# Performance work log

Hardware: AMD Instinct MI355X
Metric: run time of the kernel (lower is better)

Reference implementation:

```python
import jax, jax.numpy as jnp
import numpy as np

IDIM = 1024
HIDDEN = 4096
N_EXPERT = 8
T = 2048


def setup_inputs() -> dict:
    key = jax.random.key(0)
    ks = jax.random.split(key, 6)
    s_in = 1.0 / np.sqrt(IDIM)
    s_h = 1.0 / np.sqrt(HIDDEN)
    return {
        "xs": jax.random.normal(ks[0], (T, IDIM), dtype=jnp.float32),
        "top_k": 2,
        # gate: Linear(idim -> n_expert, bias=False); torch weight (E, D)
        "Wg": jax.random.uniform(ks[1], (N_EXPERT, IDIM), jnp.float32, -s_in, s_in),
        # experts stacked: w_1 Linear(idim->hidden), w_2 Linear(hidden->idim)
        "W1": jax.random.uniform(ks[2], (N_EXPERT, IDIM, HIDDEN), jnp.float32, -s_in, s_in),
        "b1": jax.random.uniform(ks[3], (N_EXPERT, HIDDEN), jnp.float32, -s_in, s_in),
        "W2": jax.random.uniform(ks[4], (N_EXPERT, HIDDEN, IDIM), jnp.float32, -s_h, s_h),
        "b2": jax.random.uniform(ks[5], (N_EXPERT, IDIM), jnp.float32, -s_h, s_h),
    }


def reference(xs, top_k, Wg, W1, b1, W2, b2):
    # Router: (T, E)
    router = xs @ Wg.T
    logits, selected = jax.lax.top_k(router, top_k)          # (T, k)
    # softmax over the top-k slot axis in fp32, cast back (matches torch)
    weights = jax.nn.softmax(logits.astype(jnp.float32), axis=-1).astype(xs.dtype)
    # combine weight per token per expert: (T, E). Tokens not routed to an
    # expert get weight 0, zeroing that expert's contribution (same math as
    # the masked gather / scatter-add in the torch loop).
    onehot = jax.nn.one_hot(selected, N_EXPERT, dtype=xs.dtype)  # (T, k, E)
    comb = jnp.einsum("tk,tke->te", weights, onehot)
    # all-expert FFN (dropout_rate = 0 -> identity)
    h = jax.nn.relu(jnp.einsum("td,edh->teh", xs, W1) + b1[None, :, :])
    y = jnp.einsum("teh,ehd->ted", h, W2) + b2[None, :, :]
    return jnp.einsum("te,ted->td", comb, y)
```

## Files before the change

kernel.cpp:

```cpp
#include <hip/hip_runtime.h>
#include <hip/hip_bf16.h>
#include <stdint.h>

#define T_TOK 2048
#define IDIM  1024
#define HID   4096
#define NE    8
#define BM    128
#define BN    128
#define BK    64
#define RMAX  5120
#define MAXTILES 40

typedef __bf16 bf16;
typedef bf16  bf16x8 __attribute__((ext_vector_type(8)));
typedef float f32x4  __attribute__((ext_vector_type(4)));

#define WS_NTILES   128
#define WS_TILE_E   192
#define WS_TILE_R   448
#define WS_TOK_E    1024
#define WS_TOK_W    17408
#define WS_ROW_TOK  33792
#define WS_ROW_W    54272
#define WS_H        131072
#define WS_MIN_FAST ((size_t)WS_H + (size_t)RMAX * (HID / 32) * 2)

__global__ __launch_bounds__(256) void k_zero_out(float4* __restrict__ a) {
    a[blockIdx.x * 256 + threadIdx.x] = make_float4(0.f, 0.f, 0.f, 0.f);
}

__global__ __launch_bounds__(256) void k_router(const float* __restrict__ xs,
                                                const float* __restrict__ Wg,
                                                int* __restrict__ tok_e,
                                                float* __restrict__ tok_w) {
    __shared__ float sWg[NE * IDIM];
    for (int i = threadIdx.x; i < NE * IDIM; i += 256) sWg[i] = Wg[i];
    __syncthreads();
    int wave = threadIdx.x >> 6, lane = threadIdx.x & 63;
    int t = blockIdx.x * 4 + wave;
    if (t >= T_TOK) return;
    float p[NE];
#pragma unroll
    for (int e = 0; e < NE; e++) p[e] = 0.f;
    for (int j = 0; j < IDIM / 64; j++) {
        float x = xs[(size_t)t * IDIM + j * 64 + lane];
#pragma unroll
        for (int e = 0; e < NE; e++)
            p[e] += x * sWg[e * IDIM + j * 64 + lane];
    }
#pragma unroll
    for (int e = 0; e < NE; e++) {
        float v = p[e];
        for (int off = 32; off > 0; off >>= 1) v += __shfl_down(v, off);
        p[e] = v;
    }
    if (lane == 0) {
        int e0 = 0; float l0 = p[0];
        for (int e = 1; e < NE; e++) if (p[e] > l0) { l0 = p[e]; e0 = e; }
        int e1 = -1; float l1 = -1e30f;
        for (int e = 0; e < NE; e++) if (e != e0 && p[e] > l1) { l1 = p[e]; e1 = e; }
        if (e1 < 0) e1 = (e0 + 1) & 7;
        float z = __expf(l1 - l0);
        tok_e[2 * t]     = e0;  tok_e[2 * t + 1] = e1;
        tok_w[2 * t]     = 1.f / (1.f + z);
        tok_w[2 * t + 1] = z / (1.f + z);
    }
}

__global__ __launch_bounds__(256) void k_setup(int* __restrict__ w,
                                               float* __restrict__ wf) {
    __shared__ int cnt[NE];
    __shared__ int cur[NE];
    int tid = threadIdx.x;
    if (tid < NE) cnt[tid] = 0;
    for (int i = tid; i < RMAX; i += 256) w[WS_ROW_TOK / 4 + i] = -1;
    __syncthreads();
    for (int i = tid; i < 2 * T_TOK; i += 256)
        atomicAdd(&cnt[w[WS_TOK_E / 4 + i]], 1);
    __syncthreads();
    if (tid == 0) {
        int off = 0, nt = 0;
        for (int e = 0; e < NE; e++) {
            cur[e] = off;
            int nb = (cnt[e] + BM - 1) / BM;
            for (int b = 0; b < nb && nt < MAXTILES; b++) {
                w[WS_TILE_E / 4 + nt] = e;
                w[WS_TILE_R / 4 + nt] = off + b * BM;
                nt++;
            }
            off += nb * BM;
        }
        w[WS_NTILES / 4] = nt;
    }
    __syncthreads();
    for (int i = tid; i < 2 * T_TOK; i += 256) {
        int e   = w[WS_TOK_E / 4 + i];
        int pos = atomicAdd(&cur[e], 1);
        if (pos < RMAX) {
            w[WS_ROW_TOK / 4 + pos] = i >> 1;
            wf[WS_ROW_W / 4 + pos]  = wf[WS_TOK_W / 4 + i];
        }
    }
}

__device__ inline uint4 pack8(float4 a, float4 b) {
    union { bf16 h[8]; uint4 u; } pk;
    pk.h[0] = (bf16)a.x; pk.h[1] = (bf16)a.y; pk.h[2] = (bf16)a.z; pk.h[3] = (bf16)a.w;
    pk.h[4] = (bf16)b.x; pk.h[5] = (bf16)b.y; pk.h[6] = (bf16)b.z; pk.h[7] = (bf16)b.w;
    return pk.u;
}
__device__ inline uint32_t pack2(float a, float b) {
    union { bf16 h[2]; uint32_t u; } pk;
    pk.h[0] = (bf16)a; pk.h[1] = (bf16)b;
    return pk.u;
}

__global__ __launch_bounds__(256) void k_ffn1(const float* __restrict__ xs,
                                              const float* __restrict__ W1,
                                              const float* __restrict__ b1,
                                              const int* __restrict__ wsi,
                                              bf16* __restrict__ H,
                                              int h0, int CW) {
    int ntiles = wsi[WS_NTILES / 4];
    int tile = blockIdx.y;
    if (tile >= ntiles) return;
    int e    = wsi[WS_TILE_E / 4 + tile];
    int row0 = wsi[WS_TILE_R / 4 + tile];
    int n0l  = blockIdx.x * BN;
    int n0g  = h0 + n0l;

    const int*   row_tok = wsi + WS_ROW_TOK / 4;
    const float* Be      = W1 + (size_t)e * IDIM * HID;
    const float* bias_e  = b1 + (size_t)e * HID;

    __shared__ bf16 sA[BM * BK];
    __shared__ bf16 sB[BN * 72];

    int t    = threadIdx.x;
    int lane = t & 63, wv = t >> 6;
    int wx = wv & 1, wy = wv >> 1;
    int lm = lane & 15, q = lane >> 4;

    int rtk[4];
#pragma unroll
    for (int i = 0; i < 4; i++) rtk[i] = row_tok[row0 + (t >> 3) + i * 32];

    f32x4 acc[4][4];
#pragma unroll
    for (int i = 0; i < 4; i++)
#pragma unroll
        for (int j = 0; j < 4; j++) acc[i][j] = (f32x4){0.f, 0.f, 0.f, 0.f};

    for (int kc = 0; kc < IDIM / BK; kc++) {
        if (kc) __syncthreads();
#pragma unroll
        for (int i = 0; i < 4; i++) {
            int u = t + i * 256;
            int row = u >> 3, k8 = (u & 7) * 8;
            uint4 v;
            if (rtk[i] >= 0) {
                const float* g = xs + (size_t)rtk[i] * IDIM + kc * BK + k8;
                v = pack8(*(const float4*)g, *(const float4*)(g + 4));
            } else v = make_uint4(0u, 0u, 0u, 0u);
            *(uint4*)&sA[row * BK + k8] = v;
        }
#pragma unroll
        for (int i = 0; i < 2; i++) {
            int u = t + i * 256;
            int noct = u & 15, kp = u >> 4;
            int k = kp * 2;
            const float* g = Be + (size_t)(kc * BK + k) * HID + n0g + noct * 8;
            float4 r0a = *(const float4*)g;
            float4 r0b = *(const float4*)(g + 4);
            float4 r1a = *(const float4*)(g + HID);
            float4 r1b = *(const float4*)(g + HID + 4);
            float a0[8] = {r0a.x, r0a.y, r0a.z, r0a.w, r0b.x, r0b.y, r0b.z, r0b.w};
            float a1[8] = {r1a.x, r1a.y, r1a.z, r1a.w, r1b.x, r1b.y, r1b.z, r1b.w};
            int kswz = k ^ ((noct & 3) * 16);
            int hwb  = noct * 8 * 72 + kswz;
#pragma unroll
            for (int j = 0; j < 8; j++)
                *(uint32_t*)&sB[hwb + j * 72] = pack2(a0[j], a1[j]);
        }
        __syncthreads();
#pragma unroll
        for (int ks = 0; ks < 2; ks++) {
            bf16x8 aF[4], bF[4];
#pragma unroll
            for (int mt = 0; mt < 4; mt++)
                aF[mt] = *(bf16x8*)&sA[(wy * 64 + mt * 16 + lm) * BK + ks * 32 + q * 8];
#pragma unroll
            for (int nt = 0; nt < 4; nt++) {
                int n  = wx * 64 + nt * 16 + lm;
                int kk = (ks * 32 + q * 8) ^ (((n >> 3) & 3) * 16);
                bF[nt] = *(bf16x8*)&sB[n * 72 + kk];
            }
#pragma unroll
            for (int mt = 0; mt < 4; mt++)
#pragma unroll
                for (int nt = 0; nt < 4; nt++)
                    acc[mt][nt] = __builtin_amdgcn_mfma_f32_16x16x32_bf16(
                        aF[mt], bF[nt], acc[mt][nt], 0, 0, 0);
        }
    }

#pragma unroll
    for (int nt = 0; nt < 4; nt++) {
        int col_l = n0l + wx * 64 + nt * 16 + lm;
        float bv  = bias_e[h0 + col_l];
#pragma unroll
        for (int mt = 0; mt < 4; mt++) {
            int rloc = wy * 64 + mt * 16 + q * 4;
#pragma unroll
            for (int r = 0; r < 4; r++) {
                float v = fmaxf(acc[mt][nt][r] + bv, 0.f);
                H[(size_t)(row0 + rloc + r) * CW + col_l] = (bf16)v;
            }
        }
    }
}

__global__ __launch_bounds__(256) void k_ffn2(const bf16* __restrict__ H,
                                              const float* __restrict__ W2,
                                              const float* __restrict__ b2,
                                              const int* __restrict__ wsi,
                                              const float* __restrict__ wsf,
                                              float* __restrict__ out,
                                              int h0, int CW, int addb) {
    int ntiles = wsi[WS_NTILES / 4];
    int tile = blockIdx.y;
    if (tile >= ntiles) return;
    int e    = wsi[WS_TILE_E / 4 + tile];
    int row0 = wsi[WS_TILE_R / 4 + tile];
    int n0   = blockIdx.x * BN;
    int kw   = CW / gridDim.z;
    int kb   = blockIdx.z * kw;

    const int*   row_tok = wsi + WS_ROW_TOK / 4;
    const float* row_w   = wsf + WS_ROW_W / 4;
    const float* Be      = W2 + (size_t)e * HID * IDIM;
    const float* bias_e  = b2 + (size_t)e * IDIM;

    __shared__ bf16 sA[BM * BK];
    __shared__ bf16 sB[BN * 72];

    int t    = threadIdx.x;
    int lane = t & 63, wv = t >> 6;
    int wx = wv & 1, wy = wv >> 1;
    int lm = lane & 15, q = lane >> 4;

    f32x4 acc[4][4];
#pragma unroll
    for (int i = 0; i < 4; i++)
#pragma unroll
        for (int j = 0; j < 4; j++) acc[i][j] = (f32x4){0.f, 0.f, 0.f, 0.f};

    int kiters = kw / BK;
    for (int kc = 0; kc < kiters; kc++) {
        if (kc) __syncthreads();
#pragma unroll
        for (int i = 0; i < 4; i++) {
            int u = t + i * 256;
            int row = u >> 3, k8 = (u & 7) * 8;
            *(uint4*)&sA[row * BK + k8] =
                *(const uint4*)&H[(size_t)(row0 + row) * CW + kb + kc * BK + k8];
        }
#pragma unroll
        for (int i = 0; i < 2; i++) {
            int u = t + i * 256;
            int noct = u & 15, kp = u >> 4;
            int k = kp * 2;
            const float* g = Be + (size_t)(h0 + kb + kc * BK + k) * IDIM + n0 + noct * 8;
            float4 r0a = *(const float4*)g;
            float4 r0b = *(const float4*)(g + 4);
            float4 r1a = *(const float4*)(g + IDIM);
            float4 r1b = *(const float4*)(g + IDIM + 4);
            float a0[8] = {r0a.x, r0a.y, r0a.z, r0a.w, r0b.x, r0b.y, r0b.z, r0b.w};
            float a1[8] = {r1a.x, r1a.y, r1a.z, r1a.w, r1b.x, r1b.y, r1b.z, r1b.w};
            int kswz = k ^ ((noct & 3) * 16);
            int hwb  = noct * 8 * 72 + kswz;
#pragma unroll
            for (int j = 0; j < 8; j++)
                *(uint32_t*)&sB[hwb + j * 72] = pack2(a0[j], a1[j]);
        }
        __syncthreads();
#pragma unroll
        for (int ks = 0; ks < 2; ks++) {
            bf16x8 aF[4], bF[4];
#pragma unroll
            for (int mt = 0; mt < 4; mt++)
                aF[mt] = *(bf16x8*)&sA[(wy * 64 + mt * 16 + lm) * BK + ks * 32 + q * 8];
#pragma unroll
            for (int nt = 0; nt < 4; nt++) {
                int n  = wx * 64 + nt * 16 + lm;
                int kk = (ks * 32 + q * 8) ^ (((n >> 3) & 3) * 16);
                bF[nt] = *(bf16x8*)&sB[n * 72 + kk];
            }
#pragma unroll
            for (int mt = 0; mt < 4; mt++)
#pragma unroll
                for (int nt = 0; nt < 4; nt++)
                    acc[mt][nt] = __builtin_amdgcn_mfma_f32_16x16x32_bf16(
                        aF[mt], bF[nt], acc[mt][nt], 0, 0, 0);
        }
    }

    int   tokr[16];
    float wr[16];
#pragma unroll
    for (int mt = 0; mt < 4; mt++)
#pragma unroll
        for (int r = 0; r < 4; r++) {
            int rg = row0 + wy * 64 + mt * 16 + q * 4 + r;
            tokr[mt * 4 + r] = row_tok[rg];
            wr[mt * 4 + r]   = row_w[rg];
        }
    int dobias = addb && (blockIdx.z == 0);
#pragma unroll
    for (int nt = 0; nt < 4; nt++) {
        int col  = n0 + wx * 64 + nt * 16 + lm;
        float bv = dobias ? bias_e[col] : 0.f;
#pragma unroll
        for (int mt = 0; mt < 4; mt++)
#pragma unroll
            for (int r = 0; r < 4; r++) {
                int tok = tokr[mt * 4 + r];
                if (tok >= 0)
                    atomicAdd(&out[(size_t)tok * IDIM + col],
                              wr[mt * 4 + r] * (acc[mt][nt][r] + bv));
            }
    }
}

__global__ __launch_bounds__(256) void k_fallback(const float* __restrict__ xs,
                                                  const float* __restrict__ Wg,
                                                  const float* __restrict__ W1,
                                                  const float* __restrict__ b1,
                                                  const float* __restrict__ W2,
                                                  const float* __restrict__ b2,
                                                  float* __restrict__ out) {
    __shared__ float xbuf[IDIM];
    __shared__ float hbuf[256];
    __shared__ float slog[NE];
    __shared__ int   sel[2];
    __shared__ float selw[2];

    int t   = blockIdx.x;
    int tid = threadIdx.x;

    for (int i = tid; i < IDIM; i += 256)
        xbuf[i] = xs[(size_t)t * IDIM + i];
    __syncthreads();
    {
        int e = tid >> 5, l = tid & 31;
        float p = 0.f;
        for (int d = l; d < IDIM; d += 32)
            p += xbuf[d] * Wg[e * IDIM + d];
        for (int off = 16; off > 0; off >>= 1) p += __shfl_down(p, off, 32);
        if (l == 0) slog[e] = p;
    }
    __syncthreads();
    if (tid == 0) {
        int e0 = 0; float l0 = slog[0];
        for (int e = 1; e < NE; e++) if (slog[e] > l0) { l0 = slog[e]; e0 = e; }
        int e1 = -1; float l1 = -1e30f;
        for (int e = 0; e < NE; e++) if (e != e0 && slog[e] > l1) { l1 = slog[e]; e1 = e; }
        if (e1 < 0) e1 = (e0 + 1) & 7;
        float z = __expf(l1 - l0);
        sel[0] = e0; sel[1] = e1;
        selw[0] = 1.f / (1.f + z);
        selw[1] = z / (1.f + z);
    }
    __syncthreads();

    float ytot[4] = {0.f, 0.f, 0.f, 0.f};
#pragma unroll
    for (int s = 0; s < 2; s++) {
        int   e = sel[s];
        float w = selw[s];
        const float* W1e = W1 + (size_t)e * IDIM * HID;
        const float* W2e = W2 + (size_t)e * HID * IDIM;
        float ys[4] = {0.f, 0.f, 0.f, 0.f};
        for (int hb = 0; hb < HID / 256; hb++) {
            int h = hb * 256 + tid;
            float acc = b1[e * HID + h];
            for (int d = 0; d < IDIM; d++)
                acc += xbuf[d] * W1e[(size_t)d * HID + h];
            __syncthreads();
            hbuf[tid] = fmaxf(acc, 0.f);
            __syncthreads();
            for (int hh = 0; hh < 256; hh++) {
                float hv = hbuf[hh];
                const float* wrow = W2e + (size_t)(hb * 256 + hh) * IDIM;
#pragma unroll
                for (int cc = 0; cc < 4; cc++)
                    ys[cc] += hv * wrow[cc * 256 + tid];
            }
        }
#pragma unroll
        for (int cc = 0; cc < 4; cc++)
            ytot[cc] += w * (ys[cc] + b2[e * IDIM + cc * 256 + tid]);
    }
#pragma unroll
    for (int cc = 0; cc < 4; cc++)
        out[(size_t)t * IDIM + cc * 256 + tid] = ytot[cc];
}

extern "C" void kernel_launch(void* const* d_in, const int* in_sizes, int n_in,
                              void* d_out, int out_size, void* d_ws, size_t ws_size,
                              hipStream_t stream) {
    int o = (n_in >= 7 && in_sizes[1] == 1) ? 1 : 0;
    const float* xs = (const float*)d_in[0];
    const float* Wg = (const float*)d_in[1 + o];
    const float* W1 = (const float*)d_in[2 + o];
    const float* b1 = (const float*)d_in[3 + o];
    const float* W2 = (const float*)d_in[4 + o];
    const float* b2 = (const float*)d_in[5 + o];
    float* out = (float*)d_out;

    if (ws_size < WS_MIN_FAST || d_ws == nullptr) {
        k_fallback<<<T_TOK, 256, 0, stream>>>(xs, Wg, W1, b1, W2, b2, out);
        return;
    }

    char*  ws  = (char*)d_ws;
    int*   wsi = (int*)d_ws;
    float* wsf = (float*)d_ws;
    bf16*  H   = (bf16*)(ws + WS_H);

    int HC = 1;
    while (HC < 32 &&
           (size_t)WS_H + (size_t)RMAX * (HID / HC) * 2 > ws_size)
        HC <<= 1;
    int CW = HID / HC;
    int SK = 4;
    while (CW / SK < BK) SK >>= 1;

    k_zero_out<<<T_TOK, 256, 0, stream>>>((float4*)out);
    k_router<<<T_TOK / 4, 256, 0, stream>>>(xs, Wg, wsi + WS_TOK_E / 4,
                                            wsf + WS_TOK_W / 4);
    k_setup<<<1, 256, 0, stream>>>(wsi, wsf);

    for (int c = 0; c < HC; c++) {
        k_ffn1<<<dim3(CW / BN, MAXTILES), 256, 0, stream>>>(
            xs, W1, b1, wsi, H, c * CW, CW);
        k_ffn2<<<dim3(IDIM / BN, MAXTILES, SK), 256, 0, stream>>>(
            H, W2, b2, wsi, wsf, out, c * CW, CW, c == 0 ? 1 : 0);
    }
}
```

Baseline: 519.8 us.

## Prefetch next K-tile into registers with double-buffered B and fuse output zeroing

Both FFN GEMM kernels now load the next K-chunk of activations and weights into registers while MFMAs run on the current chunk. The B tile is double-buffered in LDS, and A is written after an extra barrier. This is meant to hide global-load latency behind compute, at the cost of more registers and two barriers per iteration. Launch bounds now request two blocks per SM, and zeroing of the output buffer moves into the router kernel, which removes one launch.

```diff
diff --git a/kernel.cpp b/kernel.cpp
--- a/kernel.cpp
+++ b/kernel.cpp
@@ -11,6 +11,7 @@
 #define BK    64
 #define RMAX  5120
 #define MAXTILES 40
+#define BNS   (BN * 72)
 
 typedef __bf16 bf16;
 typedef bf16  bf16x8 __attribute__((ext_vector_type(8)));
@@ -26,14 +27,28 @@
 #define WS_H        131072
 #define WS_MIN_FAST ((size_t)WS_H + (size_t)RMAX * (HID / 32) * 2)
 
-__global__ __launch_bounds__(256) void k_zero_out(float4* __restrict__ a) {
-    a[blockIdx.x * 256 + threadIdx.x] = make_float4(0.f, 0.f, 0.f, 0.f);
+__device__ inline uint4 pack8(float4 a, float4 b) {
+    union { bf16 h[8]; uint4 u; } pk;
+    pk.h[0] = (bf16)a.x; pk.h[1] = (bf16)a.y; pk.h[2] = (bf16)a.z; pk.h[3] = (bf16)a.w;
+    pk.h[4] = (bf16)b.x; pk.h[5] = (bf16)b.y; pk.h[6] = (bf16)b.z; pk.h[7] = (bf16)b.w;
+    return pk.u;
+}
+__device__ inline uint32_t pack2(float a, float b) {
+    union { bf16 h[2]; uint32_t u; } pk;
+    pk.h[0] = (bf16)a; pk.h[1] = (bf16)b;
+    return pk.u;
 }
 
 __global__ __launch_bounds__(256) void k_router(const float* __restrict__ xs,
                                                 const float* __restrict__ Wg,
                                                 int* __restrict__ tok_e,
-                                                float* __restrict__ tok_w) {
+                                                float* __restrict__ tok_w,
+                                                float4* __restrict__ out4) {
+    int zbase = blockIdx.x * 256 + threadIdx.x;
+#pragma unroll
+    for (int i = 0; i < 4; i++)
+        out4[zbase + i * (T_TOK / 4 * 256)] = make_float4(0.f, 0.f, 0.f, 0.f);
+
     __shared__ float sWg[NE * IDIM];
     for (int i = threadIdx.x; i < NE * IDIM; i += 256) sWg[i] = Wg[i];
     __syncthreads();
@@ -104,24 +119,12 @@
     }
 }
 
-__device__ inline uint4 pack8(float4 a, float4 b) {
-    union { bf16 h[8]; uint4 u; } pk;
-    pk.h[0] = (bf16)a.x; pk.h[1] = (bf16)a.y; pk.h[2] = (bf16)a.z; pk.h[3] = (bf16)a.w;
-    pk.h[4] = (bf16)b.x; pk.h[5] = (bf16)b.y; pk.h[6] = (bf16)b.z; pk.h[7] = (bf16)b.w;
-    return pk.u;
-}
-__device__ inline uint32_t pack2(float a, float b) {
-    union { bf16 h[2]; uint32_t u; } pk;
-    pk.h[0] = (bf16)a; pk.h[1] = (bf16)b;
-    return pk.u;
-}
-
-__global__ __launch_bounds__(256) void k_ffn1(const float* __restrict__ xs,
-                                              const float* __restrict__ W1,
-                                              const float* __restrict__ b1,
-                                              const int* __restrict__ wsi,
-                                              bf16* __restrict__ H,
-                                              int h0, int CW) {
+__global__ __launch_bounds__(256, 2) void k_ffn1(const float* __restrict__ xs,
+                                                 const float* __restrict__ W1,
+                                                 const float* __restrict__ b1,
+                                                 const int* __restrict__ wsi,
+                                                 bf16* __restrict__ H,
+                                                 int h0, int CW) {
     int ntiles = wsi[WS_NTILES / 4];
     int tile = blockIdx.y;
     if (tile >= ntiles) return;
@@ -135,55 +138,83 @@
     const float* bias_e  = b1 + (size_t)e * HID;
 
     __shared__ bf16 sA[BM * BK];
-    __shared__ bf16 sB[BN * 72];
+    __shared__ bf16 sB[2][BNS];
 
     int t    = threadIdx.x;
     int lane = t & 63, wv = t >> 6;
     int wx = wv & 1, wy = wv >> 1;
     int lm = lane & 15, q = lane >> 4;
+    int noct0 = t & 15, kp0 = t >> 4;
+    int k8 = (t & 7) * 8;
 
     int rtk[4];
 #pragma unroll
     for (int i = 0; i < 4; i++) rtk[i] = row_tok[row0 + (t >> 3) + i * 32];
 
+    float4 ar[4][2];
+    float4 br[2][4];
+
+#define F1_LOADA(kc)                                                         \
+    {                                                                        \
+        _Pragma("unroll") for (int i = 0; i < 4; i++) {                      \
+            if (rtk[i] >= 0) {                                               \
+                const float* g = xs + (size_t)rtk[i] * IDIM + (kc) * BK + k8;\
+                ar[i][0] = *(const float4*)g;                                \
+                ar[i][1] = *(const float4*)(g + 4);                          \
+            } else {                                                         \
+                ar[i][0] = make_float4(0.f, 0.f, 0.f, 0.f);                  \
+                ar[i][1] = make_float4(0.f, 0.f, 0.f, 0.f);                  \
+            }                                                                \
+        }                                                                    \
+    }
+#define F1_LOADB(kc)                                                         \
+    {                                                                        \
+        _Pragma("unroll") for (int i = 0; i < 2; i++) {                      \
+            int kp = kp0 + i * 16;                                           \
+            const float* g = Be + (size_t)((kc) * BK + 2 * kp) * HID + n0g + noct0 * 8; \
+            br[i][0] = *(const float4*)g;                                    \
+            br[i][1] = *(const float4*)(g + 4);                              \
+            br[i][2] = *(const float4*)(g + HID);                            \
+            br[i][3] = *(const float4*)(g + HID + 4);                        \
+        }                                                                    \
+    }
+#define F1_WRITEA()                                                          \
+    {                                                                        \
+        _Pragma("unroll") for (int i = 0; i < 4; i++) {                      \
+            int rowA = (t >> 3) + i * 32;                                    \
+            *(uint4*)&sA[rowA * BK + k8] = pack8(ar[i][0], ar[i][1]);        \
+        }                                                                    \
+    }
+#define F1_WRITEB(buf)                                                       \
+    {                                                                        \
+        _Pragma("unroll") for (int i = 0; i < 2; i++) {                      \
+            int kp = kp0 + i * 16;                                           \
+            float a0[8] = {br[i][0].x, br[i][0].y, br[i][0].z, br[i][0].w,   \
+                           br[i][1].x, br[i][1].y, br[i][1].z, br[i][1].w};  \
+            float a1[8] = {br[i][2].x, br[i][2].y, br[i][2].z, br[i][2].w,   \
+                           br[i][3].x, br[i][3].y, br[i][3].z, br[i][3].w};  \
+            int kswz = (2 * kp) ^ ((noct0 & 3) * 16);                        \
+            int hwb  = noct0 * 8 * 72 + kswz;                                \
+            _Pragma("unroll") for (int j = 0; j < 8; j++)                    \
+                *(uint32_t*)&sB[buf][hwb + j * 72] = pack2(a0[j], a1[j]);    \
+        }                                                                    \
+    }
+
     f32x4 acc[4][4];
 #pragma unroll
     for (int i = 0; i < 4; i++)
 #pragma unroll
         for (int j = 0; j < 4; j++) acc[i][j] = (f32x4){0.f, 0.f, 0.f, 0.f};
 
-    for (int kc = 0; kc < IDIM / BK; kc++) {
-        if (kc) __syncthreads();
-#pragma unroll
-        for (int i = 0; i < 4; i++) {
-            int u = t + i * 256;
-            int row = u >> 3, k8 = (u & 7) * 8;
-            uint4 v;
-            if (rtk[i] >= 0) {
-                const float* g = xs + (size_t)rtk[i] * IDIM + kc * BK + k8;
-                v = pack8(*(const float4*)g, *(const float4*)(g + 4));
-            } else v = make_uint4(0u, 0u, 0u, 0u);
-            *(uint4*)&sA[row * BK + k8] = v;
-        }
-#pragma unroll
-        for (int i = 0; i < 2; i++) {
-            int u = t + i * 256;
-            int noct = u & 15, kp = u >> 4;
-            int k = kp * 2;
-            const float* g = Be + (size_t)(kc * BK + k) * HID + n0g + noct * 8;
-            float4 r0a = *(const float4*)g;
-            float4 r0b = *(const float4*)(g + 4);
-            float4 r1a = *(const float4*)(g + HID);
-            float4 r1b = *(const float4*)(g + HID + 4);
-            float a0[8] = {r0a.x, r0a.y, r0a.z, r0a.w, r0b.x, r0b.y, r0b.z, r0b.w};
-            float a1[8] = {r1a.x, r1a.y, r1a.z, r1a.w, r1b.x, r1b.y, r1b.z, r1b.w};
-            int kswz = k ^ ((noct & 3) * 16);
-            int hwb  = noct * 8 * 72 + kswz;
-#pragma unroll
-            for (int j = 0; j < 8; j++)
-                *(uint32_t*)&sB[hwb + j * 72] = pack2(a0[j], a1[j]);
-        }
-        __syncthreads();
+    const int KI = IDIM / BK;
+    F1_LOADA(0) F1_LOADB(0)
+    F1_WRITEA() F1_WRITEB(0)
+    __syncthreads();
+
+    for (int kc = 0; kc < KI; kc++) {
+        bool hn = (kc + 1 < KI);
+        if (hn) { F1_LOADA(kc + 1) F1_LOADB(kc + 1) }
+        const bf16* sbc = &sB[kc & 1][0];
 #pragma unroll
         for (int ks = 0; ks < 2; ks++) {
             bf16x8 aF[4], bF[4];
@@ -194,7 +225,7 @@
             for (int nt = 0; nt < 4; nt++) {
                 int n  = wx * 64 + nt * 16 + lm;
                 int kk = (ks * 32 + q * 8) ^ (((n >> 3) & 3) * 16);
-                bF[nt] = *(bf16x8*)&sB[n * 72 + kk];
+                bF[nt] = *(bf16x8*)&sbc[n * 72 + kk];
             }
 #pragma unroll
             for (int mt = 0; mt < 4; mt++)
@@ -203,6 +234,10 @@
                     acc[mt][nt] = __builtin_amdgcn_mfma_f32_16x16x32_bf16(
                         aF[mt], bF[nt], acc[mt][nt], 0, 0, 0);
         }
+        if (hn) F1_WRITEB((kc + 1) & 1)
+        __syncthreads();
+        if (hn) F1_WRITEA()
+        __syncthreads();
     }
 
 #pragma unroll
@@ -221,13 +256,13 @@
     }
 }
 
-__global__ __launch_bounds__(256) void k_ffn2(const bf16* __restrict__ H,
-                                              const float* __restrict__ W2,
-                                              const float* __restrict__ b2,
-                                              const int* __restrict__ wsi,
-                                              const float* __restrict__ wsf,
-                                              float* __restrict__ out,
-                                              int h0, int CW, int addb) {
+__global__ __launch_bounds__(256, 2) void k_ffn2(const bf16* __restrict__ H,
+                                                 const float* __restrict__ W2,
+                                                 const float* __restrict__ b2,
+                                                 const int* __restrict__ wsi,
+                                                 const float* __restrict__ wsf,
+                                                 float* __restrict__ out,
+                                                 int h0, int CW, int addb) {
     int ntiles = wsi[WS_NTILES / 4];
     int tile = blockIdx.y;
     if (tile >= ntiles) return;
@@ -243,12 +278,57 @@
     const float* bias_e  = b2 + (size_t)e * IDIM;
 
     __shared__ bf16 sA[BM * BK];
-    __shared__ bf16 sB[BN * 72];
+    __shared__ bf16 sB[2][BNS];
 
     int t    = threadIdx.x;
     int lane = t & 63, wv = t >> 6;
     int wx = wv & 1, wy = wv >> 1;
     int lm = lane & 15, q = lane >> 4;
+    int noct0 = t & 15, kp0 = t >> 4;
+    int k8 = (t & 7) * 8;
+
+    uint4  ar[4];
+    float4 br[2][4];
+
+#define F2_LOADA(kc)                                                         \
+    {                                                                        \
+        _Pragma("unroll") for (int i = 0; i < 4; i++) {                      \
+            int rowA = (t >> 3) + i * 32;                                    \
+            ar[i] = *(const uint4*)&H[(size_t)(row0 + rowA) * CW + kb + (kc) * BK + k8]; \
+        }                                                                    \
+    }
+#define F2_LOADB(kc)                                                         \
+    {                                                                        \
+        _Pragma("unroll") for (int i = 0; i < 2; i++) {                      \
+            int kp = kp0 + i * 16;                                           \
+            const float* g = Be + (size_t)(h0 + kb + (kc) * BK + 2 * kp) * IDIM + n0 + noct0 * 8; \
+            br[i][0] = *(const float4*)g;                                    \
+            br[i][1] = *(const float4*)(g + 4);                              \
+            br[i][2] = *(const float4*)(g + IDIM);                           \
+            br[i][3] = *(const float4*)(g + IDIM + 4);                       \
+        }                                                                    \
+    }
+#define F2_WRITEA()                                                          \
+    {                                                                        \
+        _Pragma("unroll") for (int i = 0; i < 4; i++) {                      \
+            int rowA = (t >> 3) + i * 32;                                    \
+            *(uint4*)&sA[rowA * BK + k8] = ar[i];                            \
+        }                                                                    \
+    }
+#define F2_WRITEB(buf)                                                       \
+    {                                                                        \
+        _Pragma("unroll") for (int i = 0; i < 2; i++) {                      \
+            int kp = kp0 + i * 16;                                           \
+            float a0[8] = {br[i][0].x, br[i][0].y, br[i][0].z, br[i][0].w,   \
+                           br[i][1].x, br[i][1].y, br[i][1].z, br[i][1].w};  \
+            float a1[8] = {br[i][2].x, br[i][2].y, br[i][2].z, br[i][2].w,   \
+                           br[i][3].x, br[i][3].y, br[i][3].z, br[i][3].w};  \
+            int kswz = (2 * kp) ^ ((noct0 & 3) * 16);                        \
+            int hwb  = noct0 * 8 * 72 + kswz;                                \
+            _Pragma("unroll") for (int j = 0; j < 8; j++)                    \
+                *(uint32_t*)&sB[buf][hwb + j * 72] = pack2(a0[j], a1[j]);    \
+        }                                                                    \
+    }
 
     f32x4 acc[4][4];
 #pragma unroll
@@ -256,35 +336,15 @@
 #pragma unroll
         for (int j = 0; j < 4; j++) acc[i][j] = (f32x4){0.f, 0.f, 0.f, 0.f};
 
-    int kiters = kw / BK;
-    for (int kc = 0; kc < kiters; kc++) {
-        if (kc) __syncthreads();
-#pragma unroll
-        for (int i = 0; i < 4; i++) {
-            int u = t + i * 256;
-            int row = u >> 3, k8 = (u & 7) * 8;
-            *(uint4*)&sA[row * BK + k8] =
-                *(const uint4*)&H[(size_t)(row0 + row) * CW + kb + kc * BK + k8];
-        }
-#pragma unroll
-        for (int i = 0; i < 2; i++) {
-            int u = t + i * 256;
-            int noct = u & 15, kp = u >> 4;
-            int k = kp * 2;
-            const float* g = Be + (size_t)(h0 + kb + kc * BK + k) * IDIM + n0 + noct * 8;
-            float4 r0a = *(const float4*)g;
-            float4 r0b = *(const float4*)(g + 4);
-            float4 r1a = *(const float4*)(g + IDIM);
-            float4 r1b = *(const float4*)(g + IDIM + 4);
-            float a0[8] = {r0a.x, r0a.y, r0a.z, r0a.w, r0b.x, r0b.y, r0b.z, r0b.w};
-            float a1[8] = {r1a.x, r1a.y, r1a.z, r1a.w, r1b.x, r1b.y, r1b.z, r1b.w};
-            int kswz = k ^ ((noct & 3) * 16);
-            int hwb  = noct * 8 * 72 + kswz;
-#pragma unroll
-            for (int j = 0; j < 8; j++)
-                *(uint32_t*)&sB[hwb + j * 72] = pack2(a0[j], a1[j]);
-        }
-        __syncthreads();
+    const int KI = kw / BK;
+    F2_LOADA(0) F2_LOADB(0)
+    F2_WRITEA() F2_WRITEB(0)
+    __syncthreads();
+
+    for (int kc = 0; kc < KI; kc++) {
+        bool hn = (kc + 1 < KI);
+        if (hn) { F2_LOADA(kc + 1) F2_LOADB(kc + 1) }
+        const bf16* sbc = &sB[kc & 1][0];
 #pragma unroll
         for (int ks = 0; ks < 2; ks++) {
             bf16x8 aF[4], bF[4];
@@ -295,7 +355,7 @@
             for (int nt = 0; nt < 4; nt++) {
                 int n  = wx * 64 + nt * 16 + lm;
                 int kk = (ks * 32 + q * 8) ^ (((n >> 3) & 3) * 16);
-                bF[nt] = *(bf16x8*)&sB[n * 72 + kk];
+                bF[nt] = *(bf16x8*)&sbc[n * 72 + kk];
             }
 #pragma unroll
             for (int mt = 0; mt < 4; mt++)
@@ -304,6 +364,10 @@
                     acc[mt][nt] = __builtin_amdgcn_mfma_f32_16x16x32_bf16(
                         aF[mt], bF[nt], acc[mt][nt], 0, 0, 0);
         }
+        if (hn) F2_WRITEB((kc + 1) & 1)
+        __syncthreads();
+        if (hn) F2_WRITEA()
+        __syncthreads();
     }
 
     int   tokr[16];
@@ -437,9 +501,8 @@
     int SK = 4;
     while (CW / SK < BK) SK >>= 1;
 
-    k_zero_out<<<T_TOK, 256, 0, stream>>>((float4*)out);
     k_router<<<T_TOK / 4, 256, 0, stream>>>(xs, Wg, wsi + WS_TOK_E / 4,
-                                            wsf + WS_TOK_W / 4);
+                                            wsf + WS_TOK_W / 4, (float4*)out);
     k_setup<<<1, 256, 0, stream>>>(wsi, wsf);
 
     for (int c = 0; c < HC; c++) {
```

New measurement: 561.5 us. 8.0% more time.
